# Performance work log

Hardware: AMD Instinct MI355X
Metric: run time of the kernel (lower is better)

## Reference

```python
import jax, jax.numpy as jnp
import numpy as np

IMAGE_W, IMAGE_H = 1024, 800
STRIDES = (8, 16, 32, 64, 128)
LEVEL_HW = ((100, 128), (50, 64), (25, 32), (13, 16), (7, 8))
TOP_N = 1000
MIN_SCORE = 0.01
NMS_THR = 0.6
MAX_DET = 100
NUM_CLASSES = 80
BATCH = 16


def _grid(h, w, stride, b):
    ys = (jnp.arange(h, dtype=jnp.float32) + 0.5) * stride
    xs = (jnp.arange(w, dtype=jnp.float32) + 0.5) * stride
    gx, gy = jnp.meshgrid(xs, ys)  # [h, w]
    pos = jnp.stack([gx, gy], axis=-1)  # [h, w, 2] = (x, y)
    return jnp.broadcast_to(pos, (b, h, w, 2))


def setup_inputs() -> dict:
    key = jax.random.key(0)
    inp = {}
    for i, ((h, w), s) in enumerate(zip(LEVEL_HW, STRIDES)):
        key, k1, k2, k3 = jax.random.split(key, 4)
        inp[f"cls{i}"] = jax.random.normal(k1, (BATCH, h, w, NUM_CLASSES), jnp.float32)
        # +3 so exp(reg) gives realistic ~20px box extents
        inp[f"reg{i}"] = jax.random.normal(k2, (BATCH, h, w, 4), jnp.float32) + 3.0
        inp[f"ctr{i}"] = jax.random.normal(k3, (BATCH, h, w, 1), jnp.float32)
        inp[f"pos{i}"] = _grid(h, w, s, BATCH)
    return inp


def _level_filter(cls, reg, ctr, pos):
    b = cls.shape[0]
    cls = jax.nn.sigmoid(cls).reshape(b, -1, NUM_CLASSES)
    reg = jnp.exp(reg).reshape(b, -1, 4)
    ctr = jax.nn.sigmoid(ctr).reshape(b, -1)
    pos = pos.reshape(b, -1, 2)
    scores = jnp.sqrt(jnp.max(cls, axis=2) * ctr)  # [b, n]
    classes = jnp.argmax(cls, axis=2)  # [b, n] int
    if scores.shape[1] >= TOP_N:
        scores, idx = jax.lax.top_k(scores, TOP_N)
        classes = jnp.take_along_axis(classes, idx, axis=1)
        reg = jnp.take_along_axis(reg, idx[..., None], axis=1)
        pos = jnp.take_along_axis(pos, idx[..., None], axis=1)
        cls = jnp.take_along_axis(cls, idx[..., None], axis=1)
    return scores, classes, reg, pos, cls


def _decode_boxes(reg, pos):
    # ltrb offsets -> x1y1x2y2, truncate to int (torch .int()), clamp to image
    xy_min = pos - reg[..., 0:2]
    xy_max = pos + reg[..., 2:4]
    bx = jnp.trunc(jnp.concatenate([xy_min, xy_max], axis=-1))
    x1 = jnp.maximum(bx[..., 0], 0.0)
    y1 = jnp.maximum(bx[..., 1], 0.0)
    x2 = jnp.minimum(bx[..., 2], IMAGE_W - 1.0)
    y2 = jnp.minimum(bx[..., 3], IMAGE_H - 1.0)
    return jnp.stack([x1, y1, x2, y2], axis=-1)


def _nms_image(scores, classes, boxes, clsp):
    valid = scores > MIN_SCORE
    order = jnp.argsort(jnp.where(valid, -scores, jnp.inf))  # valid, desc score first
    s = scores[order]
    c = classes[order].astype(jnp.float32)
    b = boxes[order]
    cp = clsp[order]
    v = valid[order]
    # pairwise IoU (keep/suppress decisions are not differentiated)
    bb = jax.lax.stop_gradient(b)
    area = (bb[:, 2] - bb[:, 0]) * (bb[:, 3] - bb[:, 1])
    lt = jnp.maximum(bb[:, None, :2], bb[None, :, :2])
    rb = jnp.minimum(bb[:, None, 2:], bb[None, :, 2:])
    wh = jnp.maximum(rb - lt, 0.0)
    inter = wh[..., 0] * wh[..., 1]
    iou = inter / (area[:, None] + area[None, :] - inter)
    n = s.shape[0]
    idxs = jnp.arange(n)

    def body(i, keep):
        sup = keep[i] & (iou[i] > NMS_THR) & (idxs > i)
        return keep & ~sup

    keep = jax.lax.fori_loop(0, n, body, v)
    rank = jnp.cumsum(keep) - 1
    slot = jnp.where(keep & (rank < MAX_DET), rank, MAX_DET)  # MAX_DET -> dropped
    out_s = jnp.full((MAX_DET,), -1.0, jnp.float32).at[slot].set(s, mode="drop")
    out_c = jnp.full((MAX_DET,), -1.0, jnp.float32).at[slot].set(c, mode="drop")
    out_b = jnp.full((MAX_DET, 4), -1.0, jnp.float32).at[slot].set(b, mode="drop")
    out_cp = jnp.full((MAX_DET, NUM_CLASSES), -1.0, jnp.float32).at[slot].set(cp, mode="drop")
    return out_s, out_c, out_b, out_cp


def reference(cls0, cls1, cls2, cls3, cls4, reg0, reg1, reg2, reg3, reg4,
              ctr0, ctr1, ctr2, ctr3, ctr4, pos0, pos1, pos2, pos3, pos4):
    clss = [cls0, cls1, cls2, cls3, cls4]
    regs = [reg0, reg1, reg2, reg3, reg4]
    ctrs = [ctr0, ctr1, ctr2, ctr3, ctr4]
    poss = [pos0, pos1, pos2, pos3, pos4]
    parts = [_level_filter(c, r, t, p) for c, r, t, p in zip(clss, regs, ctrs, poss)]
    scores = jnp.concatenate([p[0] for p in parts], axis=1)
    classes = jnp.concatenate([p[1] for p in parts], axis=1)
    reg = jnp.concatenate([p[2] for p in parts], axis=1)
    pos = jnp.concatenate([p[3] for p in parts], axis=1)
    clsp = jnp.concatenate([p[4] for p in parts], axis=1)
    boxes = _decode_boxes(reg, pos)
    return jax.vmap(_nms_image)(scores, classes, boxes, clsp)
```

## Files before the change

### kernel.cpp

```cpp
#include <hip/hip_runtime.h>
#include <math.h>

#define TOTAL_G 17064
#define BATCHN  16
#define ALLF    0xFFFFFFFFFFFFFFFFull
#define INVALID_HI 0xC3DC28F5u

typedef unsigned long long u64;
typedef unsigned int u32;
typedef unsigned short u16;

#define KEYS0_OFF   0
#define KEYS1_OFF   1638400
#define KEYS234_OFF 2048000
#define CLSI_OFF    2187264
#define NC_OFF      2733312
#define T512_OFF    2733824
#define KR_OFF      2733952
#define MSK_OFF     2799488
#define SLOTK_OFF   3323776
#define K512_OFF    3336576

struct Ptrs {
  const float *cls0,*cls1,*cls2,*cls3,*cls4;
  const float *reg0,*reg1,*reg2,*reg3,*reg4;
  const float *ctr0,*ctr1,*ctr2,*ctr3,*ctr4;
  const float *pos0,*pos1,*pos2,*pos3,*pos4;
  char *ws;
};

__device__ __forceinline__ float sigd(float x) {
  return (float)(1.0 / (1.0 + exp(-(double)x)));
}
__device__ __forceinline__ float dexp(float x) {
  return (float)exp((double)x);
}
__device__ __forceinline__ void levinfo(int gid, int& lev, int& idx, int& nl) {
  if      (gid < 12800) { lev=0; idx=gid;        nl=12800; }
  else if (gid < 16000) { lev=1; idx=gid-12800;  nl=3200;  }
  else if (gid < 16800) { lev=2; idx=gid-16000;  nl=800;   }
  else if (gid < 17008) { lev=3; idx=gid-16800;  nl=208;   }
  else                  { lev=4; idx=gid-17008;  nl=56;    }
}

__device__ __forceinline__ u64* krank_of(char* ws, int b) {
  return (u64*)(ws + KR_OFF + (size_t)b * 4096);
}
__device__ __forceinline__ u64* msk_of(char* ws, int b) {
  return (u64*)(ws + MSK_OFF + (size_t)b * 32768);
}
__device__ __forceinline__ u64* slotkey_of(char* ws, int b) {
  return (u64*)(ws + SLOTK_OFF + (size_t)b * 800);
}
__device__ __forceinline__ u64* k512_of(char* ws, int b) {
  return (u64*)(ws + K512_OFF + (size_t)b * 4096);
}

__device__ __forceinline__ float4 decode_box(const Ptrs& P, int b, int gid) {
  int lev, idx, nl; levinfo(gid, lev, idx, nl);
  const float *rp, *pp;
  if      (lev == 0) { rp = P.reg0; pp = P.pos0; }
  else if (lev == 1) { rp = P.reg1; pp = P.pos1; }
  else if (lev == 2) { rp = P.reg2; pp = P.pos2; }
  else if (lev == 3) { rp = P.reg3; pp = P.pos3; }
  else               { rp = P.reg4; pp = P.pos4; }
  float4 rv = *(const float4*)(rp + (size_t)(b * nl + idx) * 4);
  float2 pv = *(const float2*)(pp + (size_t)(b * nl + idx) * 2);
  float e0 = dexp(rv.x), e1 = dexp(rv.y), e2 = dexp(rv.z), e3 = dexp(rv.w);
  float x1 = truncf(pv.x - e0), y1 = truncf(pv.y - e1);
  float x2 = truncf(pv.x + e2), y2 = truncf(pv.y + e3);
  x1 = fmaxf(x1, 0.0f); y1 = fmaxf(y1, 0.0f);
  x2 = fminf(x2, 1023.0f); y2 = fminf(y2, 799.0f);
  return make_float4(x1, y1, x2, y2);
}

__global__ __launch_bounds__(256) void k_score(Ptrs P) {
  __shared__ float4 sk4[64 * 20];
  int b = blockIdx.y;
  int tid = threadIdx.x;
  int p0 = blockIdx.x * 64;

  #pragma unroll
  for (int it = 0; it < 5; ++it) {
    int t4 = it * 256 + tid;
    int g = p0 + t4 / 20;
    if (g < TOTAL_G) {
      int sub = t4 - (t4 / 20) * 20;
      int lev, idx, nl; levinfo(g, lev, idx, nl);
      const float* clsb;
      if      (lev == 0) clsb = P.cls0;
      else if (lev == 1) clsb = P.cls1;
      else if (lev == 2) clsb = P.cls2;
      else if (lev == 3) clsb = P.cls3;
      else               clsb = P.cls4;
      sk4[t4] = ((const float4*)(clsb + (size_t)(b * nl + idx) * 80))[sub];
    }
  }
  __syncthreads();

  int lp = tid >> 2, q = tid & 3;
  int g = p0 + lp;
  if (g >= TOTAL_G) return;

  const float4* my4 = &sk4[lp * 20 + q * 5];
  float m = -INFINITY, m2 = -INFINITY; int mi = 0;
  #pragma unroll
  for (int k = 0; k < 5; ++k) {
    float4 v = my4[k];
    int base = q * 20 + 4 * k;
    if (v.x > m) { m2 = m; m = v.x; mi = base+0; } else if (v.x > m2) m2 = v.x;
    if (v.y > m) { m2 = m; m = v.y; mi = base+1; } else if (v.y > m2) m2 = v.y;
    if (v.z > m) { m2 = m; m = v.z; mi = base+2; } else if (v.z > m2) m2 = v.z;
    if (v.w > m) { m2 = m; m = v.w; mi = base+3; } else if (v.w > m2) m2 = v.w;
  }
  #pragma unroll
  for (int xw = 1; xw <= 2; xw <<= 1) {
    float om  = __shfl_xor(m,  xw);
    float om2 = __shfl_xor(m2, xw);
    int   omi = __shfl_xor(mi, xw);
    bool take = (om > m) || (om == m && omi < mi);
    float lm  = take ? m : om;
    float wm2 = take ? om2 : m2;
    if (take) { m = om; mi = omi; }
    m2 = fmaxf(lm, wm2);
  }

  float thr = fminf(m - 1e-3f, 9.0f);
  float pmax; int ci;
  if (m2 >= thr) {
    float pv = -1.0f; int pi = 0x7fffffff;
    #pragma unroll 1
    for (int k = 0; k < 5; ++k) {
      float4 v = my4[k];
      float xs[4] = {v.x, v.y, v.z, v.w};
      #pragma unroll
      for (int e = 0; e < 4; ++e) {
        if (xs[e] >= thr) {
          float p = sigd(xs[e]);
          if (p > pv) { pv = p; pi = q * 20 + 4 * k + e; }
        }
      }
    }
    #pragma unroll
    for (int xw = 1; xw <= 2; xw <<= 1) {
      float ov = __shfl_xor(pv, xw);
      int   oi = __shfl_xor(pi, xw);
      if (ov > pv || (ov == pv && oi < pi)) { pv = ov; pi = oi; }
    }
    pmax = pv; ci = pi;
  } else {
    pmax = sigd(m); ci = mi;
  }

  if (q == 0) {
    int lev, idx, nl; levinfo(g, lev, idx, nl);
    const float* ctrb;
    if      (lev == 0) ctrb = P.ctr0;
    else if (lev == 1) ctrb = P.ctr1;
    else if (lev == 2) ctrb = P.ctr2;
    else if (lev == 3) ctrb = P.ctr3;
    else               ctrb = P.ctr4;
    float tc = ctrb[(size_t)b * nl + idx];
    float csig = sigd(tc);
    float prod = pmax * csig;
    float s = (float)sqrt((double)prod);
    ((u16*)(P.ws + CLSI_OFF))[(size_t)b * TOTAL_G + g] = (u16)ci;
    unsigned hi = ~__float_as_uint(s);
    u64 key = ((u64)hi << 15) | (unsigned)g;
    if      (lev == 0) ((u64*)(P.ws + KEYS0_OFF))  [(size_t)b * 12800 + idx] = key;
    else if (lev == 1) ((u64*)(P.ws + KEYS1_OFF))  [(size_t)b * 3200  + idx] = key;
    else               ((u64*)(P.ws + KEYS234_OFF))[(size_t)b * 1088  + (g - 16000)] = key;
  }
}

__device__ __forceinline__ u64 loadkey(const Ptrs& P, int b, int u) {
  if (u < 12800) return ((const u64*)(P.ws + KEYS0_OFF))  [(size_t)b * 12800 + u];
  if (u < 16000) return ((const u64*)(P.ws + KEYS1_OFF))  [(size_t)b * 3200  + (u - 12800)];
  return               ((const u64*)(P.ws + KEYS234_OFF))[(size_t)b * 1088  + (u - 16000)];
}
__device__ __forceinline__ ulonglong2 loadkey2(const Ptrs& P, int b, int u) {
  if (u < 12800) return *(const ulonglong2*)((const u64*)(P.ws + KEYS0_OFF)   + (size_t)b * 12800 + u);
  if (u < 16000) return *(const ulonglong2*)((const u64*)(P.ws + KEYS1_OFF)   + (size_t)b * 3200  + (u - 12800));
  return               *(const ulonglong2*)((const u64*)(P.ws + KEYS234_OFF) + (size_t)b * 1088  + (u - 16000));
}
__device__ __forceinline__ bool keep_pred(u64 k, int u, u64 T0, u64 T1) {
  bool valid = (u32)(k >> 15) < INVALID_HI;
  bool sel = (u < 12800) ? (k <= T0) : ((u < 16000) ? (k <= T1) : true);
  return valid && sel;
}

__global__ __launch_bounds__(1024) void k_prep(Ptrs P) {
  __shared__ u32 h[4][4096];
  __shared__ int wbase[144];
  __shared__ u64 sBoundary;
  __shared__ int sN5;
  int b = blockIdx.x;
  int tid = threadIdx.x, wid = tid >> 6, lane = tid & 63;
  int rep = wid & 3;
  char* ws = P.ws;

  for (int i = tid; i < 4 * 4096; i += 1024) (&h[0][0])[i] = 0;
  __syncthreads();
  for (int it = 0; it < 9; ++it) {
    int u = it * 2048 + tid * 2;
    if (u >= TOTAL_G) break;
    ulonglong2 kk = loadkey2(P, b, u);
    if ((u32)(kk.x >> 15) < INVALID_HI)
      atomicAdd(&h[rep][(u32)(kk.x >> 29) & 0xFFF], 1u);
    if (u + 1 < TOTAL_G && (u32)(kk.y >> 15) < INVALID_HI)
      atomicAdd(&h[rep][(u32)(kk.y >> 29) & 0xFFF], 1u);
  }
  __syncthreads();
  for (int i = tid; i < 4096; i += 1024)
    h[0][i] = h[0][i] + h[1][i] + h[2][i] + h[3][i];
  __syncthreads();

  if (wid == 0) {
    u32 ssum = 0;
    #pragma unroll 8
    for (int i = 0; i < 64; ++i) {
      int ii = (i + lane) & 63;
      ssum += h[0][(lane << 6) + ii];
    }
    u32 inc = ssum;
    for (int o = 1; o < 64; o <<= 1) { u32 v = __shfl_up(inc, o); if (lane >= o) inc += v; }
    u64 ball = __ballot(inc >= 512u);
    if (!ball) {
      if (lane == 0) sBoundary = ((u64)INVALID_HI << 15);
    } else {
      int Wq = __ffsll(ball) - 1;
      u32 cumBefore = __shfl(inc - ssum, Wq);
      u32 v2 = h[0][(Wq << 6) + lane];
      u32 inc2 = v2;
      for (int o = 1; o < 64; o <<= 1) { u32 x = __shfl_up(inc2, o); if (lane >= o) inc2 += x; }
      u64 ball2 = __ballot(cumBefore + inc2 >= 512u);
      int l2 = __ffsll(ball2) - 1;
      if (lane == 0) {
        int d = (Wq << 6) + l2;
        sBoundary = (48ull << 41) | ((u64)d << 29);
      }
    }
  }
  __syncthreads();
  u64 Boundary = sBoundary;
  if (tid == 0) ((u64*)(ws + T512_OFF))[b] = Boundary - 1;

  for (int it = 0; it < 9; ++it) {
    int u = it * 2048 + tid * 2;
    ulonglong2 kk = loadkey2(P, b, u);
    bool k0 = (u     < TOTAL_G) && ((u32)(kk.x >> 15) < INVALID_HI) && (kk.x < Boundary);
    bool k1 = (u + 1 < TOTAL_G) && ((u32)(kk.y >> 15) < INVALID_HI) && (kk.y < Boundary);
    u64 b0 = __ballot(k0), b1 = __ballot(k1);
    if (lane == 0) wbase[it * 16 + wid] = __popcll(b0) + __popcll(b1);
  }
  __syncthreads();
  if (wid == 0) {
    int carry = 0;
    for (int base = 0; base < 144; base += 64) {
      int idx = base + lane;
      int v = (idx < 144) ? wbase[idx] : 0;
      int inc = v;
      for (int o = 1; o < 64; o <<= 1) { int x = __shfl_up(inc, o); if (lane >= o) inc += x; }
      if (idx < 144) wbase[idx] = inc - v + carry;
      carry += __shfl(inc, 63);
    }
    if (lane == 0) sN5 = carry;
  }
  __syncthreads();
  if (tid == 0) ((int*)(ws + NC_OFF))[16 + b] = sN5;

  u64* k5 = k512_of(ws, b);
  for (int it = 0; it < 9; ++it) {
    int u = it * 2048 + tid * 2;
    ulonglong2 kk = loadkey2(P, b, u);
    bool k0 = (u     < TOTAL_G) && ((u32)(kk.x >> 15) < INVALID_HI) && (kk.x < Boundary);
    bool k1 = (u + 1 < TOTAL_G) && ((u32)(kk.y >> 15) < INVALID_HI) && (kk.y < Boundary);
    u64 b0 = __ballot(k0), b1 = __ballot(k1);
    u64 lm = (1ull << lane) - 1ull;
    int pos0 = wbase[it * 16 + wid] + __popcll(b0 & lm) + __popcll(b1 & lm);
    int pos1 = pos0 + (k0 ? 1 : 0);
    if (k0) k5[pos0] = kk.x;
    if (k1) k5[pos1] = kk.y;
  }
}

__global__ __launch_bounds__(1024) void k_mask(Ptrs P) {
  __shared__ u64 skey[512];
  __shared__ float4 sbox[512];
  __shared__ u16 srank[512];
  __shared__ u16 parts[1024];
  __shared__ u64 smaskR[4096];
  int qi = blockIdx.x, b = blockIdx.y;
  int tid = threadIdx.x;
  char* ws = P.ws;
  int n512 = ((int*)(ws + NC_OFF))[16 + b];
  const u64* k5 = k512_of(ws, b);

  if (tid < 512) {
    if (tid < n512) {
      u64 k = k5[tid];
      skey[tid] = k;
      sbox[tid] = decode_box(P, b, (int)(k & 0x7FFF));
    } else {
      skey[tid] = (ALLF - 511) + (u64)tid;
      sbox[tid] = make_float4(-1e30f, -1e30f, -1e30f, -1e30f);
    }
  }
  for (int i = tid; i < 512 * 8; i += 1024) smaskR[i] = 0ull;
  __syncthreads();

  {
    int t2 = tid & 511, half = tid >> 9;
    u64 mykey = skey[t2];
    int jb = half << 8, cnt = 0;
    #pragma unroll 4
    for (int j = jb; j < jb + 256; ++j) cnt += (skey[j] < mykey) ? 1 : 0;
    parts[tid] = (u16)cnt;
  }
  __syncthreads();
  if (tid < 512) srank[tid] = (u16)(parts[tid] + parts[tid + 512]);
  __syncthreads();

  int i = qi * 128 + (tid >> 3);
  int w = tid & 7;
  float4 bi = sbox[i];
  u64 ki = skey[i];
  int ri = srank[i];
  float ia = (bi.z - bi.x) * (bi.w - bi.y);
  #pragma unroll 8
  for (int bj = 0; bj < 64; ++bj) {
    int jj = (bj + w) & 63;
    int j = (w << 6) | jj;
    u64 kj = skey[j];
    if (ki < kj) {
      float4 bj4 = sbox[j];
      float ja  = (bj4.z - bj4.x) * (bj4.w - bj4.y);
      float ltx = fmaxf(bi.x, bj4.x), lty = fmaxf(bi.y, bj4.y);
      float rbx = fminf(bi.z, bj4.z), rby = fminf(bi.w, bj4.w);
      float wv = fmaxf(rbx - ltx, 0.0f), hv = fmaxf(rby - lty, 0.0f);
      float inter = wv * hv;
      float iou = inter / (ia + ja - inter);
      if (iou > 0.6f) {
        int rj = srank[j];
        atomicOr(&smaskR[ri * 8 + (rj >> 6)], 1ull << (rj & 63));
      }
    }
  }
  __syncthreads();

  {
    int il = tid >> 3, ww = tid & 7;
    int ig = qi * 128 + il;
    if (ig < n512) {
      int r = srank[ig];
      msk_of(ws, b)[r * 8 + ww] = smaskR[r * 8 + ww];
      if (ww == 0) krank_of(ws, b)[r] = skey[ig];
    }
  }
}

__device__ u64 select256(const u64* keys, int n, int t0, u32* hist, u64* shP, int* shT) {
  u64 Pfx = 3; int t = t0;
  const int SS[4] = {33, 21, 9, 0};
  const int WW[4] = {12, 12, 12, 9};
  for (int p = 0; p < 4; ++p) {
    int s = SS[p], wb = WW[p];
    u32 dmask = (1u << wb) - 1u;
    for (int i = threadIdx.x; i < 4096; i += 256) hist[i] = 0;
    __syncthreads();
    for (int i = threadIdx.x; i < n; i += 256) {
      u64 k = keys[i];
      if ((k >> (s + wb)) == Pfx) atomicAdd(&hist[(u32)(k >> s) & dmask], 1u);
    }
    __syncthreads();
    if (threadIdx.x < 64) {
      int lane = threadIdx.x;
      u32 ssum = 0;
      for (int i = 0; i < 64; ++i) ssum += hist[(lane << 6) + ((i + lane) & 63)];
      u32 inc = ssum;
      for (int o = 1; o < 64; o <<= 1) { u32 v = __shfl_up(inc, o); if (lane >= o) inc += v; }
      u64 ball = __ballot(inc >= (u32)t);
      int Wq = __ffsll(ball) - 1;
      u32 cumBefore = __shfl(inc - ssum, Wq);
      u32 v2 = hist[(Wq << 6) + lane];
      u32 inc2 = v2;
      for (int o = 1; o < 64; o <<= 1) { u32 x = __shfl_up(inc2, o); if (lane >= o) inc2 += x; }
      u64 ball2 = __ballot(cumBefore + inc2 >= (u32)t);
      int l2 = __ffsll(ball2) - 1;
      u32 cumB2 = __shfl(cumBefore + inc2 - v2, l2);
      if (lane == 0) { *shP = (Pfx << wb) | (u32)((Wq << 6) + l2); *shT = t - (int)cumB2; }
    }
    __syncthreads();
    Pfx = *shP; t = *shT;
    __syncthreads();
  }
  return Pfx;
}

__global__ __launch_bounds__(256) void k_reduce(Ptrs P) {
  __shared__ u64 smask[4096];
  __shared__ u32 keeplist[100];
  __shared__ int keptS;
  __shared__ u64 liveC[267];
  __shared__ union UF {
    u32 hist[4096];
    struct { u64 pk[256]; int pc[256]; float4 fkb[100]; } F;
  } UF_;
  __shared__ u64 shP; __shared__ int shT;
  __shared__ u64 bk; __shared__ int bc2;

  int b = blockIdx.x;
  int tid = threadIdx.x;
  char* ws = P.ws;
  int n512 = ((int*)(ws + NC_OFF))[16 + b];
  const u64* kr = krank_of(ws, b);

  const u64* gmask = msk_of(ws, b);
  for (int t = tid; t < 4096; t += 256) smask[t] = gmask[t];
  __syncthreads();

  if (tid < 64) {
    int lane = tid;
    u64 lw = 0;
    if (lane < 8) {
      int lo = lane << 6;
      int c = n512 - lo; if (c < 0) c = 0; if (c > 64) c = 64;
      lw = (c >= 64) ? ALLF : ((c > 0) ? ((1ull << c) - 1ull) : 0ull);
    }
    int kept = 0;
    while (kept < 100) {
      bool nz = (lane < 8) && (lw != 0ull);
      u64 bal = __ballot(nz);
      if (!bal) break;
      int W = __ffsll(bal) - 1;
      u64 wv = __shfl(lw, W);
      int bit = __ffsll(wv) - 1;
      int i = (W << 6) + bit;
      if (lane == 0) keeplist[kept] = (u32)i;
      kept++;
      if (lane == W) lw &= ~(1ull << bit);
      if (kept == 100) break;
      if (lane < 8) lw &= ~smask[i * 8 + lane];
    }
    if (lane == 0) keptS = kept;
  }
  __syncthreads();
  int kept = keptS;
  int keptW = kept;

  if (kept < 100) {
    u64 T0 = select256((const u64*)(ws + KEYS0_OFF) + (size_t)b * 12800, 12800, 1000,
                       UF_.hist, &shP, &shT);
    u64 T1 = select256((const u64*)(ws + KEYS1_OFF) + (size_t)b * 3200, 3200, 1000,
                       UF_.hist, &shP, &shT);
    u64 T512 = ((u64*)(ws + T512_OFF))[b];
    for (int w = tid; w < 267; w += 256) {
      int lo = w << 6;
      u64 m = 0;
      for (int e = 0; e < 64; ++e) {
        int u = lo + e;
        if (u < TOTAL_G) {
          u64 k = loadkey(P, b, u);
          if (keep_pred(k, u, T0, T1) && k > T512) m |= (1ull << e);
        }
      }
      liveC[w] = m;
    }
    if (tid < kept) UF_.F.fkb[tid] = decode_box(P, b, (int)(kr[keeplist[tid]] & 0x7FFF));
    __syncthreads();

    for (int k2 = 0; k2 < kept; ++k2) {
      float4 bi = UF_.F.fkb[k2];
      float ia = (bi.z - bi.x) * (bi.w - bi.y);
      for (int u = tid; u < TOTAL_G; u += 256) {
        if (!((liveC[u >> 6] >> (u & 63)) & 1ull)) continue;
        float4 bj4 = decode_box(P, b, u);
        float ja  = (bj4.z - bj4.x) * (bj4.w - bj4.y);
        float ltx = fmaxf(bi.x, bj4.x), lty = fmaxf(bi.y, bj4.y);
        float rbx = fminf(bi.z, bj4.z), rby = fminf(bi.w, bj4.w);
        float wv = fmaxf(rbx - ltx, 0.0f), hv = fmaxf(rby - lty, 0.0f);
        float inter = wv * hv;
        float iou = inter / (ia + ja - inter);
        if (iou > 0.6f) atomicAnd(&liveC[u >> 6], ~(1ull << (u & 63)));
      }
    }
    __syncthreads();

    while (kept < 100) {
      u64 mymin = ALLF; int myc = -1;
      for (int u = tid; u < TOTAL_G; u += 256) {
        if (!((liveC[u >> 6] >> (u & 63)) & 1ull)) continue;
        u64 k = loadkey(P, b, u);
        if (k < mymin) { mymin = k; myc = u; }
      }
      UF_.F.pk[tid] = mymin; UF_.F.pc[tid] = myc;
      __syncthreads();
      if (tid < 64) {
        u64 m = UF_.F.pk[tid]; int c0 = UF_.F.pc[tid];
        #pragma unroll
        for (int o = 64; o < 256; o += 64)
          if (UF_.F.pk[tid + o] < m) { m = UF_.F.pk[tid + o]; c0 = UF_.F.pc[tid + o]; }
        for (int o = 32; o > 0; o >>= 1) {
          u64 om = __shfl_down(m, o); int oc = __shfl_down(c0, o);
          if (om < m) { m = om; c0 = oc; }
        }
        if (tid == 0) { bk = m; bc2 = c0; }
      }
      __syncthreads();
      if (bk == ALLF) break;
      int cs = bc2;
      if (tid == 0) {
        slotkey_of(ws, b)[kept] = bk;
        atomicAnd(&liveC[cs >> 6], ~(1ull << (cs & 63)));
      }
      __syncthreads();
      kept++;
      if (kept == 100) break;
      float4 bi = decode_box(P, b, cs);
      float ia = (bi.z - bi.x) * (bi.w - bi.y);
      for (int u = tid; u < TOTAL_G; u += 256) {
        if (!((liveC[u >> 6] >> (u & 63)) & 1ull)) continue;
        float4 bj4 = decode_box(P, b, u);
        float ja  = (bj4.z - bj4.x) * (bj4.w - bj4.y);
        float ltx = fmaxf(bi.x, bj4.x), lty = fmaxf(bi.y, bj4.y);
        float rbx = fminf(bi.z, bj4.z), rby = fminf(bi.w, bj4.w);
        float wv = fmaxf(rbx - ltx, 0.0f), hv = fmaxf(rby - lty, 0.0f);
        float inter = wv * hv;
        float iou = inter / (ia + ja - inter);
        if (iou > 0.6f) atomicAnd(&liveC[u >> 6], ~(1ull << (u & 63)));
      }
      __syncthreads();
    }
  }

  if (tid < 100) {
    if (tid < keptW)      slotkey_of(ws, b)[tid] = kr[keeplist[tid]];
    else if (tid >= kept) slotkey_of(ws, b)[tid] = ALLF;
  }
}

__global__ __launch_bounds__(256) void k_out(Ptrs P, float* out) {
  int b = blockIdx.x, part = blockIdx.y;
  int s0 = part * 10;
  int tid = threadIdx.x;
  const u64* skl = slotkey_of(P.ws, b);

  if (tid < 10) {
    int s = s0 + tid;
    u64 key = skl[s];
    float os = -1.0f, oc = -1.0f;
    float4 bx = make_float4(-1.0f, -1.0f, -1.0f, -1.0f);
    if (key != ALLF) {
      int gid = (int)(key & 0x7FFF);
      os = __uint_as_float(~(u32)(key >> 15));
      oc = (float)((u16*)(P.ws + CLSI_OFF))[(size_t)b * TOTAL_G + gid];
      bx = decode_box(P, b, gid);
    }
    out[b * 100 + s] = os;
    out[1600 + b * 100 + s] = oc;
    *(float4*)(out + 3200 + (size_t)(b * 100 + s) * 4) = bx;
  }

  for (int t = tid; t < 800; t += 256) {
    int sl = t / 80, k = t - sl * 80;
    int s = s0 + sl;
    u64 key = skl[s];
    float val = -1.0f;
    if (key != ALLF) {
      int gid = (int)(key & 0x7FFF);
      int lev, idx, nl; levinfo(gid, lev, idx, nl);
      const float* cp;
      if      (lev == 0) cp = P.cls0;
      else if (lev == 1) cp = P.cls1;
      else if (lev == 2) cp = P.cls2;
      else if (lev == 3) cp = P.cls3;
      else               cp = P.cls4;
      val = sigd(cp[(size_t)(b * nl + idx) * 80 + k]);
    }
    out[9600 + (size_t)(b * 100 + s) * 80 + k] = val;
  }
}

extern "C" void kernel_launch(void* const* d_in, const int* in_sizes, int n_in,
                              void* d_out, int out_size, void* d_ws, size_t ws_size,
                              hipStream_t stream) {
  (void)in_sizes; (void)n_in; (void)out_size; (void)ws_size;
  Ptrs P;
  P.cls0 = (const float*)d_in[0];  P.reg0 = (const float*)d_in[1];
  P.ctr0 = (const float*)d_in[2];  P.pos0 = (const float*)d_in[3];
  P.cls1 = (const float*)d_in[4];  P.reg1 = (const float*)d_in[5];
  P.ctr1 = (const float*)d_in[6];  P.pos1 = (const float*)d_in[7];
  P.cls2 = (const float*)d_in[8];  P.reg2 = (const float*)d_in[9];
  P.ctr2 = (const float*)d_in[10]; P.pos2 = (const float*)d_in[11];
  P.cls3 = (const float*)d_in[12]; P.reg3 = (const float*)d_in[13];
  P.ctr3 = (const float*)d_in[14]; P.pos3 = (const float*)d_in[15];
  P.cls4 = (const float*)d_in[16]; P.reg4 = (const float*)d_in[17];
  P.ctr4 = (const float*)d_in[18]; P.pos4 = (const float*)d_in[19];
  P.ws = (char*)d_ws;

  k_score<<<dim3(267, 16), 256, 0, stream>>>(P);
  k_prep<<<16, 1024, 0, stream>>>(P);
  k_mask<<<dim3(4, 16), 1024, 0, stream>>>(P);
  k_reduce<<<16, 256, 0, stream>>>(P);
  k_out<<<dim3(16, 10), 256, 0, stream>>>(P, (float*)d_out);
}
```

Measured before the change: 96.06 us.

## Fuse top-512 candidate selection into the IoU mask kernel

Merges k_prep into k_mask. Each of the four query blocks per image now recomputes the histogram threshold and compaction itself and writes the selected keys straight into shared memory, with the histogram sharing a union with the mask buffers. This drops one kernel launch and the global round-trip through the k512 buffer, at the cost of doing the selection work four times per image.

```diff
diff --git a/kernel.cpp b/kernel.cpp
--- a/kernel.cpp
+++ b/kernel.cpp
@@ -19,7 +19,6 @@
 #define KR_OFF      2733952
 #define MSK_OFF     2799488
 #define SLOTK_OFF   3323776
-#define K512_OFF    3336576
 
 struct Ptrs {
   const float *cls0,*cls1,*cls2,*cls3,*cls4;
@@ -51,9 +50,6 @@
 }
 __device__ __forceinline__ u64* slotkey_of(char* ws, int b) {
   return (u64*)(ws + SLOTK_OFF + (size_t)b * 800);
-}
-__device__ __forceinline__ u64* k512_of(char* ws, int b) {
-  return (u64*)(ws + K512_OFF + (size_t)b * 4096);
 }
 
 __device__ __forceinline__ float4 decode_box(const Ptrs& P, int b, int gid) {
@@ -189,30 +185,35 @@
   return valid && sel;
 }
 
-__global__ __launch_bounds__(1024) void k_prep(Ptrs P) {
-  __shared__ u32 h[4][4096];
+__global__ __launch_bounds__(1024) void k_mask(Ptrs P) {
+  __shared__ union USh {
+    u32 H[4][4096];
+    struct { float4 sbox[512]; u64 smaskR[4096]; u16 parts[1024]; } M;
+  } U;
+  __shared__ u64 skey[512];
+  __shared__ u16 srank[512];
   __shared__ int wbase[144];
+  __shared__ int sN5;
   __shared__ u64 sBoundary;
-  __shared__ int sN5;
-  int b = blockIdx.x;
+  int qi = blockIdx.x, b = blockIdx.y;
   int tid = threadIdx.x, wid = tid >> 6, lane = tid & 63;
   int rep = wid & 3;
   char* ws = P.ws;
 
-  for (int i = tid; i < 4 * 4096; i += 1024) (&h[0][0])[i] = 0;
+  for (int i = tid; i < 4 * 4096; i += 1024) (&U.H[0][0])[i] = 0;
   __syncthreads();
   for (int it = 0; it < 9; ++it) {
     int u = it * 2048 + tid * 2;
     if (u >= TOTAL_G) break;
     ulonglong2 kk = loadkey2(P, b, u);
     if ((u32)(kk.x >> 15) < INVALID_HI)
-      atomicAdd(&h[rep][(u32)(kk.x >> 29) & 0xFFF], 1u);
+      atomicAdd(&U.H[rep][(u32)(kk.x >> 29) & 0xFFF], 1u);
     if (u + 1 < TOTAL_G && (u32)(kk.y >> 15) < INVALID_HI)
-      atomicAdd(&h[rep][(u32)(kk.y >> 29) & 0xFFF], 1u);
+      atomicAdd(&U.H[rep][(u32)(kk.y >> 29) & 0xFFF], 1u);
   }
   __syncthreads();
   for (int i = tid; i < 4096; i += 1024)
-    h[0][i] = h[0][i] + h[1][i] + h[2][i] + h[3][i];
+    U.H[0][i] = U.H[0][i] + U.H[1][i] + U.H[2][i] + U.H[3][i];
   __syncthreads();
 
   if (wid == 0) {
@@ -220,7 +221,7 @@
     #pragma unroll 8
     for (int i = 0; i < 64; ++i) {
       int ii = (i + lane) & 63;
-      ssum += h[0][(lane << 6) + ii];
+      ssum += U.H[0][(lane << 6) + ii];
     }
     u32 inc = ssum;
     for (int o = 1; o < 64; o <<= 1) { u32 v = __shfl_up(inc, o); if (lane >= o) inc += v; }
@@ -230,7 +231,7 @@
     } else {
       int Wq = __ffsll(ball) - 1;
       u32 cumBefore = __shfl(inc - ssum, Wq);
-      u32 v2 = h[0][(Wq << 6) + lane];
+      u32 v2 = U.H[0][(Wq << 6) + lane];
       u32 inc2 = v2;
       for (int o = 1; o < 64; o <<= 1) { u32 x = __shfl_up(inc2, o); if (lane >= o) inc2 += x; }
       u64 ball2 = __ballot(cumBefore + inc2 >= 512u);
@@ -243,7 +244,7 @@
   }
   __syncthreads();
   u64 Boundary = sBoundary;
-  if (tid == 0) ((u64*)(ws + T512_OFF))[b] = Boundary - 1;
+  if (qi == 0 && tid == 0) ((u64*)(ws + T512_OFF))[b] = Boundary - 1;
 
   for (int it = 0; it < 9; ++it) {
     int u = it * 2048 + tid * 2;
@@ -267,9 +268,9 @@
     if (lane == 0) sN5 = carry;
   }
   __syncthreads();
-  if (tid == 0) ((int*)(ws + NC_OFF))[16 + b] = sN5;
-
-  u64* k5 = k512_of(ws, b);
+  int n512 = sN5;
+  if (qi == 0 && tid == 0) ((int*)(ws + NC_OFF))[16 + b] = n512;
+
   for (int it = 0; it < 9; ++it) {
     int u = it * 2048 + tid * 2;
     ulonglong2 kk = loadkey2(P, b, u);
@@ -279,34 +280,20 @@
     u64 lm = (1ull << lane) - 1ull;
     int pos0 = wbase[it * 16 + wid] + __popcll(b0 & lm) + __popcll(b1 & lm);
     int pos1 = pos0 + (k0 ? 1 : 0);
-    if (k0) k5[pos0] = kk.x;
-    if (k1) k5[pos1] = kk.y;
-  }
-}
-
-__global__ __launch_bounds__(1024) void k_mask(Ptrs P) {
-  __shared__ u64 skey[512];
-  __shared__ float4 sbox[512];
-  __shared__ u16 srank[512];
-  __shared__ u16 parts[1024];
-  __shared__ u64 smaskR[4096];
-  int qi = blockIdx.x, b = blockIdx.y;
-  int tid = threadIdx.x;
-  char* ws = P.ws;
-  int n512 = ((int*)(ws + NC_OFF))[16 + b];
-  const u64* k5 = k512_of(ws, b);
+    if (k0) skey[pos0] = kk.x;
+    if (k1) skey[pos1] = kk.y;
+  }
+  __syncthreads();
 
   if (tid < 512) {
     if (tid < n512) {
-      u64 k = k5[tid];
-      skey[tid] = k;
-      sbox[tid] = decode_box(P, b, (int)(k & 0x7FFF));
+      U.M.sbox[tid] = decode_box(P, b, (int)(skey[tid] & 0x7FFF));
     } else {
       skey[tid] = (ALLF - 511) + (u64)tid;
-      sbox[tid] = make_float4(-1e30f, -1e30f, -1e30f, -1e30f);
-    }
-  }
-  for (int i = tid; i < 512 * 8; i += 1024) smaskR[i] = 0ull;
+      U.M.sbox[tid] = make_float4(-1e30f, -1e30f, -1e30f, -1e30f);
+    }
+  }
+  for (int i = tid; i < 512 * 8; i += 1024) U.M.smaskR[i] = 0ull;
   __syncthreads();
 
   {
@@ -315,15 +302,15 @@
     int jb = half << 8, cnt = 0;
     #pragma unroll 4
     for (int j = jb; j < jb + 256; ++j) cnt += (skey[j] < mykey) ? 1 : 0;
-    parts[tid] = (u16)cnt;
-  }
-  __syncthreads();
-  if (tid < 512) srank[tid] = (u16)(parts[tid] + parts[tid + 512]);
+    U.M.parts[tid] = (u16)cnt;
+  }
+  __syncthreads();
+  if (tid < 512) srank[tid] = (u16)(U.M.parts[tid] + U.M.parts[tid + 512]);
   __syncthreads();
 
   int i = qi * 128 + (tid >> 3);
   int w = tid & 7;
-  float4 bi = sbox[i];
+  float4 bi = U.M.sbox[i];
   u64 ki = skey[i];
   int ri = srank[i];
   float ia = (bi.z - bi.x) * (bi.w - bi.y);
@@ -333,7 +320,7 @@
     int j = (w << 6) | jj;
     u64 kj = skey[j];
     if (ki < kj) {
-      float4 bj4 = sbox[j];
+      float4 bj4 = U.M.sbox[j];
       float ja  = (bj4.z - bj4.x) * (bj4.w - bj4.y);
       float ltx = fmaxf(bi.x, bj4.x), lty = fmaxf(bi.y, bj4.y);
       float rbx = fminf(bi.z, bj4.z), rby = fminf(bi.w, bj4.w);
@@ -342,7 +329,7 @@
       float iou = inter / (ia + ja - inter);
       if (iou > 0.6f) {
         int rj = srank[j];
-        atomicOr(&smaskR[ri * 8 + (rj >> 6)], 1ull << (rj & 63));
+        atomicOr(&U.M.smaskR[ri * 8 + (rj >> 6)], 1ull << (rj & 63));
       }
     }
   }
@@ -353,7 +340,7 @@
     int ig = qi * 128 + il;
     if (ig < n512) {
       int r = srank[ig];
-      msk_of(ws, b)[r * 8 + ww] = smaskR[r * 8 + ww];
+      msk_of(ws, b)[r * 8 + ww] = U.M.smaskR[r * 8 + ww];
       if (ww == 0) krank_of(ws, b)[r] = skey[ig];
     }
   }
@@ -599,7 +586,6 @@
   P.ws = (char*)d_ws;
 
   k_score<<<dim3(267, 16), 256, 0, stream>>>(P);
-  k_prep<<<16, 1024, 0, stream>>>(P);
   k_mask<<<dim3(4, 16), 1024, 0, stream>>>(P);
   k_reduce<<<16, 256, 0, stream>>>(P);
   k_out<<<dim3(16, 10), 256, 0, stream>>>(P, (float*)d_out);
```

New measurement: 94.38 us. No clear change (-1.7%).
